# Kernel tuning notes

Hardware: AMD Instinct MI355X
Metric: run time of the kernel (lower is better)

The kernel has to match this reference:

```python
import jax, jax.numpy as jnp
import numpy as np
import math

HIST_LEN = 101          # int(pattern_window / 0.001) + 1 = int(0.1/0.001)+1
MAX_PAT_LEN = 10        # config.max_pattern_length
KERNEL_SIZE = 10        # min(20, max_pattern_length)
NUM_KERNELS = 5
EPS = 1e-6

def _make_kernels():
    # Faithful to _create_correlation_kernels
    t = np.arange(KERNEL_SIZE, dtype=np.float32)
    k = np.zeros((NUM_KERNELS, KERNEL_SIZE), dtype=np.float32)
    k[0] = np.exp(-t / 5.0)                                   # exponential decay
    center = KERNEL_SIZE // 2
    sigma = KERNEL_SIZE // 4
    k[1] = np.exp(-(t - center) ** 2 / (2.0 * sigma ** 2))    # gaussian
    k[2] = np.sin(2.0 * math.pi * 0.5 * t / KERNEL_SIZE)      # sine
    k[3] = t / KERNEL_SIZE                                    # ramp
    k[4, 0] = 1.0                                             # delta
    return jnp.asarray(k)

def setup_inputs() -> dict:
    key = jax.random.key(0)
    ks = jax.random.split(key, 4)
    B, D, P = 256, 8192, 1024
    return {
        "input_spikes": jax.random.normal(ks[0], (B, D), jnp.float32),
        "spike_history": jax.random.normal(ks[1], (HIST_LEN, D), jnp.float32),
        "pattern_templates": jax.random.normal(ks[2], (P, MAX_PAT_LEN, D), jnp.float32),
        "pattern_weights": jax.random.normal(ks[3], (P, D), jnp.float32),
        "correlation_kernels": _make_kernels(),
        "history_index": 95,
        "current_time": 1,
    }

def reference(input_spikes, spike_history, pattern_templates, pattern_weights,
              correlation_kernels, history_index, current_time):
    # Circular-buffer write of the first batch element (stateful buffer update)
    hist_idx = history_index % HIST_LEN
    hist = spike_history.at[hist_idx].set(input_spikes[0])

    W = min(MAX_PAT_LEN, HIST_LEN)          # recent_window = 10
    recent = hist[-W:]                      # [W, D]
    templ = pattern_templates[:, :W]        # [P, W, D]
    K = correlation_kernels[:, :W]          # [5, W]
    K2 = K * K

    # numerator_{p,k,d} = sum_w K[k,w]^2 * recent[w,d] * templ[p,w,d]
    num = jnp.einsum('kw,wd,pwd->pkd', K2, recent, templ)
    rnorm = jnp.sqrt(jnp.einsum('kw,wd->kd', K2, recent * recent)) + EPS   # [5, D]
    tnorm = jnp.sqrt(jnp.einsum('kw,pwd->pkd', K2, templ * templ)) + EPS   # [P, 5, D]
    corr = num / (rnorm[None] * tnorm)      # [P, 5, D]

    # torch: per-kernel mean over D, then mean over the 5 kernels == mean over (k, d)
    strength = corr.mean(axis=(1, 2))       # [P]

    acts = strength[None, :] + input_spikes @ pattern_weights.T  # [B, P]
    return jax.nn.sigmoid(acts)
```

## Files before the change

kernel.cpp:

```cpp
#include <hip/hip_runtime.h>
#include <math.h>

#define DCOL 8192
#define PNUM 1024
#define BATCH 256
#define HISTLEN 101
#define WIN 10
#define NK 5
#define EPSF 1e-6f
#define SLICES 8
#define SLICE_COLS (DCOL/SLICES)
#define PPB 4
#define BKK 32

#define WS_RECENT 0
#define WS_RINV   (WIN*DCOL)
#define WS_PSTR   (WS_RINV + NK*DCOL)
#define WS_K2     (WS_PSTR + SLICES*PNUM)
#define WS_PART   131584

typedef __attribute__((ext_vector_type(8))) short bf16x8;
typedef __attribute__((ext_vector_type(4))) float f32x4;

__device__ inline short f2bf_s(float x) {
  union { float f; unsigned u; } c; c.f = x;
  unsigned r = c.u + 0x7FFFu + ((c.u >> 16) & 1u);
  return (short)(r >> 16);
}
__device__ inline float bf2f_s(short b) {
  union { unsigned u; float f; } c; c.u = ((unsigned)(unsigned short)b) << 16;
  return c.f;
}

__global__ __launch_bounds__(256) void k0_prep(
    const float* __restrict__ spikes, const float* __restrict__ hist,
    const float* __restrict__ ck, const int* __restrict__ hidxp,
    float* __restrict__ ws)
{
  const int g = blockIdx.x * 256 + threadIdx.x;
  const int col = g * 4;
  int hidx = hidxp[0] % HISTLEN;
  if (hidx < 0) hidx += HISTLEN;

  if (blockIdx.x == 0 && threadIdx.x < NK*WIN) {
    const float v = ck[threadIdx.x];
    ws[WS_K2 + threadIdx.x] = v * v;
  }

  float k2[NK][WIN];
#pragma unroll
  for (int k = 0; k < NK; ++k)
#pragma unroll
    for (int w = 0; w < WIN; ++w) { float v = ck[k*WIN + w]; k2[k][w] = v * v; }

  float rn[NK][4];
#pragma unroll
  for (int k = 0; k < NK; ++k)
#pragma unroll
    for (int j = 0; j < 4; ++j) rn[k][j] = 0.f;

#pragma unroll
  for (int w = 0; w < WIN; ++w) {
    const int row = HISTLEN - WIN + w;
    const float* src = (row == hidx) ? spikes : (hist + (size_t)row * DCOL);
    const float4 r = *(const float4*)(src + col);
    *(float4*)(ws + WS_RECENT + w*DCOL + col) = r;
    const float rr[4] = { r.x, r.y, r.z, r.w };
#pragma unroll
    for (int k = 0; k < NK; ++k)
#pragma unroll
      for (int j = 0; j < 4; ++j) rn[k][j] += k2[k][w] * rr[j] * rr[j];
  }

#pragma unroll
  for (int k = 0; k < NK; ++k) {
    float o[4];
#pragma unroll
    for (int j = 0; j < 4; ++j) o[j] = 1.0f / (sqrtf(rn[k][j]) + EPSF);
    float4 v; v.x = o[0]; v.y = o[1]; v.z = o[2]; v.w = o[3];
    *(float4*)(ws + WS_RINV + k*DCOL + col) = v;
  }
}

__global__ __launch_bounds__(256) void k1_strength(
    const float* __restrict__ templ, const float* __restrict__ wk2,
    const float* __restrict__ recent, const float* __restrict__ rinv,
    float* __restrict__ pstr)
{
  __shared__ float red[PPB][4];
  const int sl  = blockIdx.x;
  const int p0  = blockIdx.y * PPB;
  const int tid = threadIdx.x;
  const int wid = tid >> 6;
  const int col = tid * 4;

  const float* __restrict__ tbase  = templ + (size_t)p0 * WIN * DCOL + sl*SLICE_COLS + col;
  const float* __restrict__ rbase  = recent + sl*SLICE_COLS + col;
  const float* __restrict__ ribase = rinv   + sl*SLICE_COLS + col;

  float4 r[WIN];
#pragma unroll
  for (int w = 0; w < WIN; ++w)
    r[w] = *(const float4*)(rbase + w*DCOL);
  float4 ri[NK];
#pragma unroll
  for (int k = 0; k < NK; ++k)
    ri[k] = *(const float4*)(ribase + k*DCOL);

  float4 tp[6];
#pragma unroll
  for (int i = 0; i < 6; ++i)
    tp[i] = *(const float4*)(tbase + (size_t)i*DCOL);

#pragma unroll
  for (int pi = 0; pi < PPB; ++pi) {
    float nj[NK][4], tj[NK][4];
#pragma unroll
    for (int k = 0; k < NK; ++k)
#pragma unroll
      for (int j = 0; j < 4; ++j) { nj[k][j] = 0.f; tj[k][j] = 0.f; }

#pragma unroll
    for (int w = 0; w < WIN; ++w) {
      const int t = pi*WIN + w;
      const float4 t4 = tp[t % 6];
      if (t + 6 < PPB*WIN)
        tp[t % 6] = *(const float4*)(tbase + (size_t)(t + 6)*DCOL);
      const float4 r4 = r[w];
      const float x[4] = { r4.x*t4.x, r4.y*t4.y, r4.z*t4.z, r4.w*t4.w };
      const float y[4] = { t4.x*t4.x, t4.y*t4.y, t4.z*t4.z, t4.w*t4.w };
#pragma unroll
      for (int k = 0; k < NK; ++k) {
        const float cf = wk2[k*WIN + w];
#pragma unroll
        for (int j = 0; j < 4; ++j) {
          nj[k][j] = fmaf(cf, x[j], nj[k][j]);
          tj[k][j] = fmaf(cf, y[j], tj[k][j]);
        }
      }
    }

    float acc[4] = {0.f, 0.f, 0.f, 0.f};
#pragma unroll
    for (int k = 0; k < NK; ++k) {
      const float rik[4] = { ri[k].x, ri[k].y, ri[k].z, ri[k].w };
#pragma unroll
      for (int j = 0; j < 4; ++j)
        acc[j] += nj[k][j] * rik[j] * rsqrtf(tj[k][j]);
    }
    float a = acc[0] + acc[1] + acc[2] + acc[3];
#pragma unroll
    for (int off = 32; off > 0; off >>= 1) a += __shfl_down(a, off, 64);
    if ((tid & 63) == 0) red[pi][wid] = a;
  }

  __syncthreads();
  if (tid < PPB) {
    const float s = red[tid][0] + red[tid][1] + red[tid][2] + red[tid][3];
    pstr[sl*PNUM + p0 + tid] = s * (1.0f / (NK * DCOL));
  }
}

__global__ __launch_bounds__(512) void k2_mfma(
    const float* __restrict__ A, const float* __restrict__ Wt,
    float* __restrict__ part, const int ksub)
{
  __shared__ short Ah[4][256][8], Al[4][256][8];
  __shared__ short Wh[4][128][8], Wl[4][128][8];

  const int sk  = blockIdx.x;
  const int bn  = blockIdx.y;
  const int tid = threadIdx.x;
  const int lane = tid & 63;
  const int wid  = tid >> 6;
  const size_t k0 = (size_t)sk * ksub;

  const int srow = tid >> 3;
  const int skc  = (tid & 7) * 4;
  const int skg  = skc >> 3;
  const int sko  = skc & 7;

  const float* Ap = A  + (size_t)srow * DCOL + k0 + skc;
  const float* Wp = Wt + (size_t)(bn*128 + srow) * DCOL + k0 + skc;

  f32x4 acc[2][8];
#pragma unroll
  for (int mt = 0; mt < 2; ++mt)
#pragma unroll
    for (int nt = 0; nt < 8; ++nt)
#pragma unroll
      for (int r = 0; r < 4; ++r) acc[mt][nt][r] = 0.f;

  const int niter = ksub / BKK;
  float4 ra[4], rw[2];
#pragma unroll
  for (int p = 0; p < 4; ++p) ra[p] = *(const float4*)(Ap + (size_t)(p*64)*DCOL);
#pragma unroll
  for (int p = 0; p < 2; ++p) rw[p] = *(const float4*)(Wp + (size_t)(p*64)*DCOL);

  for (int it = 0; it < niter; ++it) {
    __syncthreads();
#pragma unroll
    for (int p = 0; p < 4; ++p) {
      const float v[4] = { ra[p].x, ra[p].y, ra[p].z, ra[p].w };
      short h[4], l[4];
#pragma unroll
      for (int j = 0; j < 4; ++j) {
        h[j] = f2bf_s(v[j]);
        l[j] = f2bf_s(v[j] - bf2f_s(h[j]));
      }
      *(short4*)&Ah[skg][srow + p*64][sko] = make_short4(h[0],h[1],h[2],h[3]);
      *(short4*)&Al[skg][srow + p*64][sko] = make_short4(l[0],l[1],l[2],l[3]);
    }
#pragma unroll
    for (int p = 0; p < 2; ++p) {
      const float v[4] = { rw[p].x, rw[p].y, rw[p].z, rw[p].w };
      short h[4], l[4];
#pragma unroll
      for (int j = 0; j < 4; ++j) {
        h[j] = f2bf_s(v[j]);
        l[j] = f2bf_s(v[j] - bf2f_s(h[j]));
      }
      *(short4*)&Wh[skg][srow + p*64][sko] = make_short4(h[0],h[1],h[2],h[3]);
      *(short4*)&Wl[skg][srow + p*64][sko] = make_short4(l[0],l[1],l[2],l[3]);
    }
    __syncthreads();
    if (it + 1 < niter) {
#pragma unroll
      for (int p = 0; p < 4; ++p)
        ra[p] = *(const float4*)(Ap + (it+1)*BKK + (size_t)(p*64)*DCOL);
#pragma unroll
      for (int p = 0; p < 2; ++p)
        rw[p] = *(const float4*)(Wp + (it+1)*BKK + (size_t)(p*64)*DCOL);
    }

    const int frow = lane & 15;
    const int fkg  = lane >> 4;
    bf16x8 wfh[8], wfl[8];
#pragma unroll
    for (int nt = 0; nt < 8; ++nt) {
      wfh[nt] = *(const bf16x8*)&Wh[fkg][nt*16 + frow][0];
      wfl[nt] = *(const bf16x8*)&Wl[fkg][nt*16 + frow][0];
    }
    bf16x8 afh[2], afl[2];
#pragma unroll
    for (int mt = 0; mt < 2; ++mt) {
      afh[mt] = *(const bf16x8*)&Ah[fkg][wid*32 + mt*16 + frow][0];
      afl[mt] = *(const bf16x8*)&Al[fkg][wid*32 + mt*16 + frow][0];
    }
#pragma unroll
    for (int mt = 0; mt < 2; ++mt)
#pragma unroll
      for (int nt = 0; nt < 8; ++nt) {
        acc[mt][nt] = __builtin_amdgcn_mfma_f32_16x16x32_bf16(
            afh[mt], wfh[nt], acc[mt][nt], 0, 0, 0);
        acc[mt][nt] = __builtin_amdgcn_mfma_f32_16x16x32_bf16(
            afh[mt], wfl[nt], acc[mt][nt], 0, 0, 0);
        acc[mt][nt] = __builtin_amdgcn_mfma_f32_16x16x32_bf16(
            afl[mt], wfh[nt], acc[mt][nt], 0, 0, 0);
      }
  }

  float* pp = part + (size_t)sk * (BATCH * PNUM);
#pragma unroll
  for (int mt = 0; mt < 2; ++mt)
#pragma unroll
    for (int nt = 0; nt < 8; ++nt) {
      const int col = bn*128 + nt*16 + (lane & 15);
#pragma unroll
      for (int r = 0; r < 4; ++r) {
        const int row = wid*32 + mt*16 + (lane >> 4)*4 + r;
        pp[(size_t)row * PNUM + col] = acc[mt][nt][r];
      }
    }
}

__global__ __launch_bounds__(256) void k3_combine(
    const float* __restrict__ part, const float* __restrict__ pstr,
    float* __restrict__ out, const int spl)
{
  const int g = blockIdx.x * 256 + threadIdx.x;
  const int i4 = g * 4;
  const int p = i4 & (PNUM - 1);
  float acc[4] = {0.f, 0.f, 0.f, 0.f};
#pragma unroll
  for (int sl = 0; sl < SLICES; ++sl) {
    const float4 s4 = *(const float4*)(pstr + sl*PNUM + p);
    acc[0]+=s4.x; acc[1]+=s4.y; acc[2]+=s4.z; acc[3]+=s4.w;
  }
  for (int s = 0; s < spl; ++s) {
    const float4 v = *(const float4*)(part + (size_t)s * (BATCH*PNUM) + i4);
    acc[0]+=v.x; acc[1]+=v.y; acc[2]+=v.z; acc[3]+=v.w;
  }
  float4 o;
  o.x = 1.f / (1.f + __expf(-acc[0]));
  o.y = 1.f / (1.f + __expf(-acc[1]));
  o.z = 1.f / (1.f + __expf(-acc[2]));
  o.w = 1.f / (1.f + __expf(-acc[3]));
  *(float4*)(out + i4) = o;
}

extern "C" void kernel_launch(void* const* d_in, const int* in_sizes, int n_in,
                              void* d_out, int out_size, void* d_ws, size_t ws_size,
                              hipStream_t stream)
{
  const float* spikes = (const float*)d_in[0];
  const float* hist   = (const float*)d_in[1];
  const float* templ  = (const float*)d_in[2];
  const float* wts    = (const float*)d_in[3];
  const float* ck     = (const float*)d_in[4];
  const int*   hidx   = (const int*)d_in[5];
  float* ws  = (float*)d_ws;
  float* out = (float*)d_out;

  int spl = 32;
  while (spl > 1 &&
         ws_size < ((size_t)WS_PART + (size_t)spl * BATCH * PNUM) * 4)
    spl >>= 1;
  const int ksub = DCOL / spl;

  k0_prep<<<dim3(8), dim3(256), 0, stream>>>(spikes, hist, ck, hidx, ws);
  k1_strength<<<dim3(SLICES, PNUM/PPB), dim3(256), 0, stream>>>(
      templ, ws + WS_K2, ws + WS_RECENT, ws + WS_RINV, ws + WS_PSTR);
  k2_mfma<<<dim3(spl, PNUM/128), dim3(512), 0, stream>>>(
      spikes, wts, ws + WS_PART, ksub);
  k3_combine<<<dim3(BATCH*PNUM/(256*4)), dim3(256), 0, stream>>>(
      ws + WS_PART, ws + WS_PSTR, out, spl);
}
```

Baseline: 104.0 us.

## Fuse strength and GEMM kernels into one interleaved launch to overlap bandwidth and MFMA

Merges the memory-bound template-correlation kernel and the split-K bf16x3 MFMA GEMM into a single launch. Block indices are interleaved two correlation blocks to one GEMM block, so both kinds of work run concurrently on the compute units. The GEMM tile shrinks from 256x128 with 512 threads to 128x64 with 256 threads, which gives more, smaller GEMM blocks. In exchange, the shared-memory and register footprint of the fused kernel is the larger of the two paths, which may lower occupancy for the correlation blocks.

New measurement: 105.4 us. About the same (+1.3%).

```diff
diff --git a/kernel.cpp b/kernel.cpp
--- a/kernel.cpp
+++ b/kernel.cpp
@@ -82,197 +82,205 @@
   }
 }
 
-__global__ __launch_bounds__(256) void k1_strength(
+__global__ __launch_bounds__(256) void k12_fused(
+    const float* __restrict__ A, const float* __restrict__ Wt,
     const float* __restrict__ templ, const float* __restrict__ wk2,
     const float* __restrict__ recent, const float* __restrict__ rinv,
-    float* __restrict__ pstr)
+    float* __restrict__ pstr, float* __restrict__ part,
+    const int spl, const int ksub, const int nk2)
 {
-  __shared__ float red[PPB][4];
-  const int sl  = blockIdx.x;
-  const int p0  = blockIdx.y * PPB;
+  __shared__ __align__(16) char smem[24576 + 64];
+  const int bid = blockIdx.x;
   const int tid = threadIdx.x;
-  const int wid = tid >> 6;
-  const int col = tid * 4;
-
-  const float* __restrict__ tbase  = templ + (size_t)p0 * WIN * DCOL + sl*SLICE_COLS + col;
-  const float* __restrict__ rbase  = recent + sl*SLICE_COLS + col;
-  const float* __restrict__ ribase = rinv   + sl*SLICE_COLS + col;
-
-  float4 r[WIN];
-#pragma unroll
-  for (int w = 0; w < WIN; ++w)
-    r[w] = *(const float4*)(rbase + w*DCOL);
-  float4 ri[NK];
-#pragma unroll
-  for (int k = 0; k < NK; ++k)
-    ri[k] = *(const float4*)(ribase + k*DCOL);
-
-  float4 tp[6];
-#pragma unroll
-  for (int i = 0; i < 6; ++i)
-    tp[i] = *(const float4*)(tbase + (size_t)i*DCOL);
-
-#pragma unroll
-  for (int pi = 0; pi < PPB; ++pi) {
-    float nj[NK][4], tj[NK][4];
+  const int q = bid / 3;
+  const int r3 = bid - q*3;
+
+  if (r3 == 2 && q < nk2) {
+    short (*Ah)[128][8] = (short(*)[128][8])(smem);
+    short (*Al)[128][8] = (short(*)[128][8])(smem + 8192);
+    short (*Wh)[64][8]  = (short(*)[64][8]) (smem + 16384);
+    short (*Wl)[64][8]  = (short(*)[64][8]) (smem + 20480);
+
+    const int sk  = q % spl;
+    const int bnm = q / spl;
+    const int bn  = bnm & 15;
+    const int bm  = bnm >> 4;
+    const int lane = tid & 63;
+    const int wid  = tid >> 6;
+    const size_t k0 = (size_t)sk * ksub;
+
+    const int srow = tid >> 3;
+    const int skc  = (tid & 7) * 4;
+    const int skg  = skc >> 3;
+    const int sko  = skc & 7;
+
+    const float* Ap = A  + (size_t)(bm*128 + srow) * DCOL + k0 + skc;
+    const float* Wp = Wt + (size_t)(bn*64  + srow) * DCOL + k0 + skc;
+
+    f32x4 acc[2][4];
+#pragma unroll
+    for (int mt = 0; mt < 2; ++mt)
+#pragma unroll
+      for (int nt = 0; nt < 4; ++nt)
+#pragma unroll
+        for (int rr = 0; rr < 4; ++rr) acc[mt][nt][rr] = 0.f;
+
+    const int niter = ksub / BKK;
+    float4 ra[4], rw[2];
+#pragma unroll
+    for (int p = 0; p < 4; ++p) ra[p] = *(const float4*)(Ap + (size_t)(p*32)*DCOL);
+#pragma unroll
+    for (int p = 0; p < 2; ++p) rw[p] = *(const float4*)(Wp + (size_t)(p*32)*DCOL);
+
+    for (int it = 0; it < niter; ++it) {
+      __syncthreads();
+#pragma unroll
+      for (int p = 0; p < 4; ++p) {
+        const float v[4] = { ra[p].x, ra[p].y, ra[p].z, ra[p].w };
+        short h[4], l[4];
+#pragma unroll
+        for (int j = 0; j < 4; ++j) {
+          h[j] = f2bf_s(v[j]);
+          l[j] = f2bf_s(v[j] - bf2f_s(h[j]));
+        }
+        *(short4*)&Ah[skg][srow + p*32][sko] = make_short4(h[0],h[1],h[2],h[3]);
+        *(short4*)&Al[skg][srow + p*32][sko] = make_short4(l[0],l[1],l[2],l[3]);
+      }
+#pragma unroll
+      for (int p = 0; p < 2; ++p) {
+        const float v[4] = { rw[p].x, rw[p].y, rw[p].z, rw[p].w };
+        short h[4], l[4];
+#pragma unroll
+        for (int j = 0; j < 4; ++j) {
+          h[j] = f2bf_s(v[j]);
+          l[j] = f2bf_s(v[j] - bf2f_s(h[j]));
+        }
+        *(short4*)&Wh[skg][srow + p*32][sko] = make_short4(h[0],h[1],h[2],h[3]);
+        *(short4*)&Wl[skg][srow + p*32][sko] = make_short4(l[0],l[1],l[2],l[3]);
+      }
+      __syncthreads();
+      if (it + 1 < niter) {
+#pragma unroll
+        for (int p = 0; p < 4; ++p)
+          ra[p] = *(const float4*)(Ap + (it+1)*BKK + (size_t)(p*32)*DCOL);
+#pragma unroll
+        for (int p = 0; p < 2; ++p)
+          rw[p] = *(const float4*)(Wp + (it+1)*BKK + (size_t)(p*32)*DCOL);
+      }
+
+      const int frow = lane & 15;
+      const int fkg  = lane >> 4;
+      bf16x8 wfh[4], wfl[4];
+#pragma unroll
+      for (int nt = 0; nt < 4; ++nt) {
+        wfh[nt] = *(const bf16x8*)&Wh[fkg][nt*16 + frow][0];
+        wfl[nt] = *(const bf16x8*)&Wl[fkg][nt*16 + frow][0];
+      }
+      bf16x8 afh[2], afl[2];
+#pragma unroll
+      for (int mt = 0; mt < 2; ++mt) {
+        afh[mt] = *(const bf16x8*)&Ah[fkg][wid*32 + mt*16 + frow][0];
+        afl[mt] = *(const bf16x8*)&Al[fkg][wid*32 + mt*16 + frow][0];
+      }
+#pragma unroll
+      for (int mt = 0; mt < 2; ++mt)
+#pragma unroll
+        for (int nt = 0; nt < 4; ++nt) {
+          acc[mt][nt] = __builtin_amdgcn_mfma_f32_16x16x32_bf16(
+              afh[mt], wfh[nt], acc[mt][nt], 0, 0, 0);
+          acc[mt][nt] = __builtin_amdgcn_mfma_f32_16x16x32_bf16(
+              afh[mt], wfl[nt], acc[mt][nt], 0, 0, 0);
+          acc[mt][nt] = __builtin_amdgcn_mfma_f32_16x16x32_bf16(
+              afl[mt], wfh[nt], acc[mt][nt], 0, 0, 0);
+        }
+    }
+
+    float* pp = part + (size_t)sk * (BATCH * PNUM);
+#pragma unroll
+    for (int mt = 0; mt < 2; ++mt)
+#pragma unroll
+      for (int nt = 0; nt < 4; ++nt) {
+        const int col = bn*64 + nt*16 + (lane & 15);
+#pragma unroll
+        for (int rr = 0; rr < 4; ++rr) {
+          const int row = bm*128 + wid*32 + mt*16 + (lane >> 4)*4 + rr;
+          pp[(size_t)row * PNUM + col] = acc[mt][nt][rr];
+        }
+      }
+  } else {
+    float (*red)[4] = (float(*)[4])(smem + 24576);
+    const int k1idx = (q < nk2) ? (q*2 + r3) : (bid - nk2);
+    const int sl  = k1idx & 7;
+    const int p0  = (k1idx >> 3) * PPB;
+    const int wid = tid >> 6;
+    const int col = tid * 4;
+
+    const float* __restrict__ tbase  = templ + (size_t)p0 * WIN * DCOL + sl*SLICE_COLS + col;
+    const float* __restrict__ rbase  = recent + sl*SLICE_COLS + col;
+    const float* __restrict__ ribase = rinv   + sl*SLICE_COLS + col;
+
+    float4 r[WIN];
+#pragma unroll
+    for (int w = 0; w < WIN; ++w)
+      r[w] = *(const float4*)(rbase + w*DCOL);
+    float4 ri[NK];
 #pragma unroll
     for (int k = 0; k < NK; ++k)
-#pragma unroll
-      for (int j = 0; j < 4; ++j) { nj[k][j] = 0.f; tj[k][j] = 0.f; }
-
-#pragma unroll
-    for (int w = 0; w < WIN; ++w) {
-      const int t = pi*WIN + w;
-      const float4 t4 = tp[t % 6];
-      if (t + 6 < PPB*WIN)
-        tp[t % 6] = *(const float4*)(tbase + (size_t)(t + 6)*DCOL);
-      const float4 r4 = r[w];
-      const float x[4] = { r4.x*t4.x, r4.y*t4.y, r4.z*t4.z, r4.w*t4.w };
-      const float y[4] = { t4.x*t4.x, t4.y*t4.y, t4.z*t4.z, t4.w*t4.w };
+      ri[k] = *(const float4*)(ribase + k*DCOL);
+
+    float4 tp[6];
+#pragma unroll
+    for (int i = 0; i < 6; ++i)
+      tp[i] = *(const float4*)(tbase + (size_t)i*DCOL);
+
+#pragma unroll
+    for (int pi = 0; pi < PPB; ++pi) {
+      float nj[NK][4], tj[NK][4];
+#pragma unroll
+      for (int k = 0; k < NK; ++k)
+#pragma unroll
+        for (int j = 0; j < 4; ++j) { nj[k][j] = 0.f; tj[k][j] = 0.f; }
+
+#pragma unroll
+      for (int w = 0; w < WIN; ++w) {
+        const int t = pi*WIN + w;
+        const float4 t4 = tp[t % 6];
+        if (t + 6 < PPB*WIN)
+          tp[t % 6] = *(const float4*)(tbase + (size_t)(t + 6)*DCOL);
+        const float4 r4 = r[w];
+        const float x[4] = { r4.x*t4.x, r4.y*t4.y, r4.z*t4.z, r4.w*t4.w };
+        const float y[4] = { t4.x*t4.x, t4.y*t4.y, t4.z*t4.z, t4.w*t4.w };
+#pragma unroll
+        for (int k = 0; k < NK; ++k) {
+          const float cf = wk2[k*WIN + w];
+#pragma unroll
+          for (int j = 0; j < 4; ++j) {
+            nj[k][j] = fmaf(cf, x[j], nj[k][j]);
+            tj[k][j] = fmaf(cf, y[j], tj[k][j]);
+          }
+        }
+      }
+
+      float acc1[4] = {0.f, 0.f, 0.f, 0.f};
 #pragma unroll
       for (int k = 0; k < NK; ++k) {
-        const float cf = wk2[k*WIN + w];
-#pragma unroll
-        for (int j = 0; j < 4; ++j) {
-          nj[k][j] = fmaf(cf, x[j], nj[k][j]);
-          tj[k][j] = fmaf(cf, y[j], tj[k][j]);
-        }
-      }
+        const float rik[4] = { ri[k].x, ri[k].y, ri[k].z, ri[k].w };
+#pragma unroll
+        for (int j = 0; j < 4; ++j)
+          acc1[j] += nj[k][j] * rik[j] * rsqrtf(tj[k][j]);
+      }
+      float a = acc1[0] + acc1[1] + acc1[2] + acc1[3];
+#pragma unroll
+      for (int off = 32; off > 0; off >>= 1) a += __shfl_down(a, off, 64);
+      if ((tid & 63) == 0) red[pi][wid] = a;
     }
 
-    float acc[4] = {0.f, 0.f, 0.f, 0.f};
-#pragma unroll
-    for (int k = 0; k < NK; ++k) {
-      const float rik[4] = { ri[k].x, ri[k].y, ri[k].z, ri[k].w };
-#pragma unroll
-      for (int j = 0; j < 4; ++j)
-        acc[j] += nj[k][j] * rik[j] * rsqrtf(tj[k][j]);
+    __syncthreads();
+    if (tid < PPB) {
+      const float s = red[tid][0] + red[tid][1] + red[tid][2] + red[tid][3];
+      pstr[sl*PNUM + p0 + tid] = s * (1.0f / (NK * DCOL));
     }
-    float a = acc[0] + acc[1] + acc[2] + acc[3];
-#pragma unroll
-    for (int off = 32; off > 0; off >>= 1) a += __shfl_down(a, off, 64);
-    if ((tid & 63) == 0) red[pi][wid] = a;
-  }
-
-  __syncthreads();
-  if (tid < PPB) {
-    const float s = red[tid][0] + red[tid][1] + red[tid][2] + red[tid][3];
-    pstr[sl*PNUM + p0 + tid] = s * (1.0f / (NK * DCOL));
-  }
-}
-
-__global__ __launch_bounds__(512) void k2_mfma(
-    const float* __restrict__ A, const float* __restrict__ Wt,
-    float* __restrict__ part, const int ksub)
-{
-  __shared__ short Ah[4][256][8], Al[4][256][8];
-  __shared__ short Wh[4][128][8], Wl[4][128][8];
-
-  const int sk  = blockIdx.x;
-  const int bn  = blockIdx.y;
-  const int tid = threadIdx.x;
-  const int lane = tid & 63;
-  const int wid  = tid >> 6;
-  const size_t k0 = (size_t)sk * ksub;
-
-  const int srow = tid >> 3;
-  const int skc  = (tid & 7) * 4;
-  const int skg  = skc >> 3;
-  const int sko  = skc & 7;
-
-  const float* Ap = A  + (size_t)srow * DCOL + k0 + skc;
-  const float* Wp = Wt + (size_t)(bn*128 + srow) * DCOL + k0 + skc;
-
-  f32x4 acc[2][8];
-#pragma unroll
-  for (int mt = 0; mt < 2; ++mt)
-#pragma unroll
-    for (int nt = 0; nt < 8; ++nt)
-#pragma unroll
-      for (int r = 0; r < 4; ++r) acc[mt][nt][r] = 0.f;
-
-  const int niter = ksub / BKK;
-  float4 ra[4], rw[2];
-#pragma unroll
-  for (int p = 0; p < 4; ++p) ra[p] = *(const float4*)(Ap + (size_t)(p*64)*DCOL);
-#pragma unroll
-  for (int p = 0; p < 2; ++p) rw[p] = *(const float4*)(Wp + (size_t)(p*64)*DCOL);
-
-  for (int it = 0; it < niter; ++it) {
-    __syncthreads();
-#pragma unroll
-    for (int p = 0; p < 4; ++p) {
-      const float v[4] = { ra[p].x, ra[p].y, ra[p].z, ra[p].w };
-      short h[4], l[4];
-#pragma unroll
-      for (int j = 0; j < 4; ++j) {
-        h[j] = f2bf_s(v[j]);
-        l[j] = f2bf_s(v[j] - bf2f_s(h[j]));
-      }
-      *(short4*)&Ah[skg][srow + p*64][sko] = make_short4(h[0],h[1],h[2],h[3]);
-      *(short4*)&Al[skg][srow + p*64][sko] = make_short4(l[0],l[1],l[2],l[3]);
-    }
-#pragma unroll
-    for (int p = 0; p < 2; ++p) {
-      const float v[4] = { rw[p].x, rw[p].y, rw[p].z, rw[p].w };
-      short h[4], l[4];
-#pragma unroll
-      for (int j = 0; j < 4; ++j) {
-        h[j] = f2bf_s(v[j]);
-        l[j] = f2bf_s(v[j] - bf2f_s(h[j]));
-      }
-      *(short4*)&Wh[skg][srow + p*64][sko] = make_short4(h[0],h[1],h[2],h[3]);
-      *(short4*)&Wl[skg][srow + p*64][sko] = make_short4(l[0],l[1],l[2],l[3]);
-    }
-    __syncthreads();
-    if (it + 1 < niter) {
-#pragma unroll
-      for (int p = 0; p < 4; ++p)
-        ra[p] = *(const float4*)(Ap + (it+1)*BKK + (size_t)(p*64)*DCOL);
-#pragma unroll
-      for (int p = 0; p < 2; ++p)
-        rw[p] = *(const float4*)(Wp + (it+1)*BKK + (size_t)(p*64)*DCOL);
-    }
-
-    const int frow = lane & 15;
-    const int fkg  = lane >> 4;
-    bf16x8 wfh[8], wfl[8];
-#pragma unroll
-    for (int nt = 0; nt < 8; ++nt) {
-      wfh[nt] = *(const bf16x8*)&Wh[fkg][nt*16 + frow][0];
-      wfl[nt] = *(const bf16x8*)&Wl[fkg][nt*16 + frow][0];
-    }
-    bf16x8 afh[2], afl[2];
-#pragma unroll
-    for (int mt = 0; mt < 2; ++mt) {
-      afh[mt] = *(const bf16x8*)&Ah[fkg][wid*32 + mt*16 + frow][0];
-      afl[mt] = *(const bf16x8*)&Al[fkg][wid*32 + mt*16 + frow][0];
-    }
-#pragma unroll
-    for (int mt = 0; mt < 2; ++mt)
-#pragma unroll
-      for (int nt = 0; nt < 8; ++nt) {
-        acc[mt][nt] = __builtin_amdgcn_mfma_f32_16x16x32_bf16(
-            afh[mt], wfh[nt], acc[mt][nt], 0, 0, 0);
-        acc[mt][nt] = __builtin_amdgcn_mfma_f32_16x16x32_bf16(
-            afh[mt], wfl[nt], acc[mt][nt], 0, 0, 0);
-        acc[mt][nt] = __builtin_amdgcn_mfma_f32_16x16x32_bf16(
-            afl[mt], wfh[nt], acc[mt][nt], 0, 0, 0);
-      }
-  }
-
-  float* pp = part + (size_t)sk * (BATCH * PNUM);
-#pragma unroll
-  for (int mt = 0; mt < 2; ++mt)
-#pragma unroll
-    for (int nt = 0; nt < 8; ++nt) {
-      const int col = bn*128 + nt*16 + (lane & 15);
-#pragma unroll
-      for (int r = 0; r < 4; ++r) {
-        const int row = wid*32 + mt*16 + (lane >> 4)*4 + r;
-        pp[(size_t)row * PNUM + col] = acc[mt][nt][r];
-      }
-    }
+  }
 }
 
 __global__ __launch_bounds__(256) void k3_combine(
@@ -318,12 +326,13 @@
          ws_size < ((size_t)WS_PART + (size_t)spl * BATCH * PNUM) * 4)
     spl >>= 1;
   const int ksub = DCOL / spl;
+  const int nk2  = spl * (BATCH/128) * (PNUM/64);
+  const int nk1  = SLICES * (PNUM/PPB);
 
   k0_prep<<<dim3(8), dim3(256), 0, stream>>>(spikes, hist, ck, hidx, ws);
-  k1_strength<<<dim3(SLICES, PNUM/PPB), dim3(256), 0, stream>>>(
-      templ, ws + WS_K2, ws + WS_RECENT, ws + WS_RINV, ws + WS_PSTR);
-  k2_mfma<<<dim3(spl, PNUM/128), dim3(512), 0, stream>>>(
-      spikes, wts, ws + WS_PART, ksub);
+  k12_fused<<<dim3(nk1 + nk2), dim3(256), 0, stream>>>(
+      spikes, wts, templ, ws + WS_K2, ws + WS_RECENT, ws + WS_RINV,
+      ws + WS_PSTR, ws + WS_PART, spl, ksub, nk2);
   k3_combine<<<dim3(BATCH*PNUM/(256*4)), dim3(256), 0, stream>>>(
       ws + WS_PART, ws + WS_PSTR, out, spl);
 }
```
